# Performance work log

Measured on AMD Instinct MI355X. Metric: run time of the kernel, lower is better.

The kernel has to match this reference:

```python
import jax, jax.numpy as jnp
import numpy as np

B, N, D, H, M, O = 8, 1024, 256, 512, 256, 256


def _mlp(x, W1, b1, W2, b2):
    # two-layer MLP: Linear -> ReLU -> Linear (torch Linear: x @ W.T + b)
    return jax.nn.relu(x @ W1.T + b1) @ W2.T + b2


def _lstm(x, W_ih, W_hh, b):
    # x: [B, N, D] -> h: [B, N, H]; single-layer unidirectional LSTM, torch gate order i,f,g,o
    Bt, Nt, _ = x.shape
    x_proj = x @ W_ih.T + b  # [B, N, 4H] precompute input projection

    def step(carry, xt):
        h, c = carry
        gates = xt + h @ W_hh.T
        i, f, g, o = jnp.split(gates, 4, axis=-1)
        i, f, o = jax.nn.sigmoid(i), jax.nn.sigmoid(f), jax.nn.sigmoid(o)
        c = f * c + i * jnp.tanh(g)
        h = o * jnp.tanh(c)
        return (h, c), h

    h0 = jnp.zeros((Bt, W_hh.shape[1]), x.dtype)
    (_, _), hs = jax.lax.scan(step, (h0, h0), jnp.swapaxes(x_proj, 0, 1))
    return jnp.swapaxes(hs, 0, 1)


def setup_inputs() -> dict:
    key = jax.random.key(0)
    ks = jax.random.split(key, 32)
    p = lambda k, s: jax.random.normal(k, s, jnp.float32) * 0.02
    inp = {
        "feats": jax.random.normal(ks[0], (B, N, D), jnp.float32),
        "adj": jax.random.randint(ks[1], (B, N, N), 0, 2, jnp.int32),
        "W_ih": p(ks[2], (4 * H, D)),
        "W_hh": p(ks[3], (4 * H, H)),
        "b_ih": jnp.zeros((4 * H,), jnp.float32),
        "b_hh": jnp.zeros((4 * H,), jnp.float32),
        "gx_W1": p(ks[4], (M, H)), "gx_b1": jnp.zeros((M,), jnp.float32),
        "gx_W2": p(ks[5], (M, M)), "gx_b2": jnp.zeros((M,), jnp.float32),
        "gz_W1": p(ks[6], (M, H)), "gz_b1": jnp.zeros((M,), jnp.float32),
        "gz_W2": p(ks[7], (M, M)), "gz_b2": jnp.zeros((M,), jnp.float32),
        "gv_W1": p(ks[8], (M, H)), "gv_b1": jnp.zeros((M,), jnp.float32),
        "gv_W2": p(ks[9], (M, M)), "gv_b2": jnp.zeros((M,), jnp.float32),
        "gn_W1": p(ks[10], (M, M)), "gn_b1": jnp.zeros((M,), jnp.float32),
        "gn_W2": p(ks[11], (O, M)), "gn_b2": jnp.zeros((O,), jnp.float32),
        "out_W": p(ks[12], (O, H + O)), "out_b": jnp.zeros((O,), jnp.float32),
    }
    return inp


def reference(feats, adj, W_ih, W_hh, b_ih, b_hh,
              gx_W1, gx_b1, gx_W2, gx_b2,
              gz_W1, gz_b1, gz_W2, gz_b2,
              gv_W1, gv_b1, gv_W2, gv_b2,
              gn_W1, gn_b1, gn_W2, gn_b2,
              out_W, out_b):
    h = _lstm(feats, W_ih, W_hh, b_ih + b_hh)  # [B, N, H]

    # Note: in the source, concat_1[:, :lstm_hidden_dim] == s_i and
    # concat_2[:, :lstm_hidden_dim] == s_j, so scores = <g_x(s_i), g_v(s_j)>
    ax = _mlp(h, gx_W1, gx_b1, gx_W2, gx_b2)  # [B, N, M]
    av = _mlp(h, gv_W1, gv_b1, gv_W2, gv_b2)  # [B, N, M]
    scores = jnp.einsum('bim,bjm->bij', ax, av)  # [B, N, N]

    eye = jnp.eye(N, dtype=bool)
    mask = (adj > 0) & ~eye[None]  # valid neighbors
    w = jax.nn.softmax(jnp.where(mask, scores, -1e30), axis=-1)
    w = w * mask  # zero out rows with no neighbors (softmax of all -inf -> uniform)

    sagg = jnp.einsum('bij,bjh->bih', w, h)  # weighted neighbor sum [B, N, H]
    agg = _mlp(_mlp(sagg, gz_W1, gz_b1, gz_W2, gz_b2), gn_W1, gn_b1, gn_W2, gn_b2)
    has_nb = mask.any(axis=-1, keepdims=True)  # [B, N, 1]
    agg = jnp.where(has_nb, agg, 0.0)  # isolated nodes get zero aggregate

    combined = jnp.concatenate([h, agg], axis=-1)  # [B, N, H+O]
    return combined @ out_W.T + out_b
```

## Files before the change

### kernel.cpp

```cpp
#include <hip/hip_runtime.h>

typedef unsigned short u16;
typedef unsigned long long u64;
using short8 = __attribute__((ext_vector_type(8))) short;
using f32x4  = __attribute__((ext_vector_type(4))) float;

#define GF_RELU  1
#define GF_F32   2
#define GF_XPOSE 4

__device__ __forceinline__ float b2f(u16 x) {
    unsigned u = ((unsigned)x) << 16;
    return __builtin_bit_cast(float, u);
}
__device__ __forceinline__ u16 f2b(float f) {
    unsigned u = __builtin_bit_cast(unsigned, f);
    unsigned r = u + 0x7FFFu + ((u >> 16) & 1u);
    return (u16)(r >> 16);
}
__device__ __forceinline__ f32x4 mfma_bf16(uint4 a, uint4 b, f32x4 c) {
    return __builtin_amdgcn_mfma_f32_16x16x32_bf16(
        __builtin_bit_cast(short8, a), __builtin_bit_cast(short8, b), c, 0, 0, 0);
}
__device__ __forceinline__ f32x4 zero4() { f32x4 z = {0.f, 0.f, 0.f, 0.f}; return z; }

__global__ __launch_bounds__(256) void cvt_bf16(const float* __restrict__ src,
                                                u16* __restrict__ dst, int n) {
    for (int i = blockIdx.x * 256 + threadIdx.x; i < n; i += gridDim.x * 256)
        dst[i] = f2b(src[i]);
}

__global__ void pack_params(const float* __restrict__ Whh, const float* __restrict__ Wih,
                            const float* __restrict__ bih, const float* __restrict__ bhh,
                            u16* __restrict__ WhhP, u16* __restrict__ WihP,
                            float* __restrict__ biasP) {
    int p = blockIdx.x;
    int t = threadIdx.x;
    int orig = ((p & 3) << 9) + (p >> 2);
    WhhP[((long)p << 9) + t]       = f2b(Whh[((long)orig << 9) + t]);
    WhhP[((long)p << 9) + 256 + t] = f2b(Whh[((long)orig << 9) + 256 + t]);
    WihP[((long)p << 8) + t]       = f2b(Wih[((long)orig << 8) + t]);
    if (t == 0) biasP[p] = bih[orig] + bhh[orig];
}

__global__ __launch_bounds__(256) void gemm_bt(
    const u16* __restrict__ A, const u16* __restrict__ A2, int ksplit,
    const u16* __restrict__ B, void* __restrict__ Cout,
    int M, int N, int K,
    long sAb, long sBb, long sCb,
    const float* __restrict__ bias, const float* __restrict__ rowmask, int flags) {
    __shared__ __align__(16) u16 As[64][40];
    __shared__ __align__(16) u16 Bs[128][40];
    const int bz = blockIdx.z;
    const u16* Ab = A + (long)bz * sAb;
    const u16* Bb = B + (long)bz * sBb;
    const int m0 = blockIdx.x << 6, n0 = blockIdx.y << 7;
    const int tid = threadIdx.x;
    const int lane = tid & 63, wave = tid >> 6;
    const int srow = tid >> 2, skc = (tid & 3) << 3;
    const int frm = lane & 15, fq = lane >> 4;

    auto loadA = [&](int ka) -> uint4 {
        const u16* p = (ka < ksplit)
            ? Ab + (long)(m0 + srow) * ksplit + ka
            : A2 + (long)(m0 + srow) * (K - ksplit) + (ka - ksplit);
        return *(const uint4*)p;
    };
    const u16* Brow0 = Bb + (long)(n0 + srow) * K;
    const u16* Brow1 = Bb + (long)(n0 + 64 + srow) * K;

    f32x4 acc[8];
#pragma unroll
    for (int i = 0; i < 8; i++) acc[i] = zero4();

    uint4 a  = loadA(skc);
    uint4 b0 = *(const uint4*)(Brow0 + skc);
    uint4 b1 = *(const uint4*)(Brow1 + skc);

    for (int k0 = 0; k0 < K; k0 += 32) {
        __syncthreads();
        *(uint4*)&As[srow][skc] = a;
        *(uint4*)&Bs[srow][skc] = b0;
        *(uint4*)&Bs[64 + srow][skc] = b1;
        __syncthreads();
        int kn = k0 + 32;
        if (kn < K) {
            a  = loadA(kn + skc);
            b0 = *(const uint4*)(Brow0 + kn + skc);
            b1 = *(const uint4*)(Brow1 + kn + skc);
        }
        uint4 af = *(const uint4*)&As[(wave << 4) + frm][fq << 3];
#pragma unroll
        for (int nt = 0; nt < 8; nt++) {
            uint4 bf = *(const uint4*)&Bs[(nt << 4) + frm][fq << 3];
            acc[nt] = mfma_bf16(af, bf, acc[nt]);
        }
    }
#pragma unroll
    for (int nt = 0; nt < 8; nt++) {
        int col = n0 + (nt << 4) + frm;
        float bv = bias ? bias[col] : 0.f;
#pragma unroll
        for (int r = 0; r < 4; r++) {
            int row = m0 + (wave << 4) + (fq << 2) + r;
            float v = acc[nt][r] + bv;
            if (flags & GF_RELU) v = fmaxf(v, 0.f);
            if (rowmask) v *= rowmask[row];
            long orow = (flags & GF_XPOSE) ? (long)((row & 1023) * 8 + (row >> 10))
                                           : (long)row;
            if (flags & GF_F32)
                ((float*)Cout)[(long)bz * sCb + orow * N + col] = v;
            else
                ((u16*)Cout)[(long)bz * sCb + orow * N + col] = f2b(v);
        }
    }
}

__global__ __launch_bounds__(512, 1) void lstm_rec(
    const u16* __restrict__ WhhP, const u16* __restrict__ xproj,
    u16* __restrict__ h, u64* __restrict__ hx) {
    __shared__ __align__(16) unsigned hshare[8][256];
    const int bid = blockIdx.x;
    const int g = bid & 7;
    const int s = bid >> 3;
    const int tid = threadIdx.x;
    const int lane = tid & 63, wv = tid >> 6;
    const int frm = lane & 15, fq = lane >> 4;
    const int colbase = (s << 8) + (wv << 5);

    uint4 bfrag[2][16];
#pragma unroll
    for (int T = 0; T < 2; T++)
#pragma unroll
        for (int kk = 0; kk < 16; kk++)
            bfrag[T][kk] = *(const uint4*)&WhhP[((long)(colbase + (T << 4) + frm) << 9) +
                                                (kk << 5) + (fq << 3)];

    unsigned* hw = &hshare[wv][0];
    float creg = 0.f;
    int budget = 1 << 20;

#pragma unroll 1
    for (int t = 0; t < 1024; t++) {
        float xp0 = b2f(xproj[((long)(t * 8 + g) << 11) + colbase + frm]);
        float xp1 = b2f(xproj[((long)(t * 8 + g) << 11) + colbase + 16 + frm]);

        float s0, s1;
        if (t > 0) {
            const u64* buf = hx + (g << 9) + (((t - 1) & 1) << 8);
            const u64* p0 = buf + lane;
            const u64* p1 = buf + 64 + lane;
            const u64* p2 = buf + 128 + lane;
            const u64* p3 = buf + 192 + lane;
            u64 v0, v1, v2, v3;
            const unsigned want = (unsigned)t;
            while (true) {
                asm volatile(
                    "global_load_dwordx2 %0, %4, off sc0 sc1\n\t"
                    "global_load_dwordx2 %1, %5, off sc0 sc1\n\t"
                    "global_load_dwordx2 %2, %6, off sc0 sc1\n\t"
                    "global_load_dwordx2 %3, %7, off sc0 sc1\n\t"
                    "s_waitcnt vmcnt(0)"
                    : "=&v"(v0), "=&v"(v1), "=&v"(v2), "=&v"(v3)
                    : "v"(p0), "v"(p1), "v"(p2), "v"(p3)
                    : "memory");
                bool ok = ((unsigned)(v0 >> 32) == want) &
                          ((unsigned)(v1 >> 32) == want) &
                          ((unsigned)(v2 >> 32) == want) &
                          ((unsigned)(v3 >> 32) == want);
                if (__all(ok) || --budget < 0) break;
            }
            hw[lane]       = (unsigned)v0;
            hw[64 + lane]  = (unsigned)v1;
            hw[128 + lane] = (unsigned)v2;
            hw[192 + lane] = (unsigned)v3;

            f32x4 a0p[4], a1p[4];
#pragma unroll
            for (int r = 0; r < 4; r++) { a0p[r] = zero4(); a1p[r] = zero4(); }
#pragma unroll
            for (int r4 = 0; r4 < 4; r4++) {
                uint4 af[4];
#pragma unroll
                for (int q = 0; q < 4; q++)
                    af[q] = *(const uint4*)&hw[(((r4 << 2) | q) << 4) + (fq << 2)];
#pragma unroll
                for (int q = 0; q < 4; q++) {
                    a0p[r4] = mfma_bf16(af[q], bfrag[0][(r4 << 2) | q], a0p[r4]);
                    a1p[r4] = mfma_bf16(af[q], bfrag[1][(r4 << 2) | q], a1p[r4]);
                }
            }
            s0 = (a0p[0][0] + a0p[1][0]) + (a0p[2][0] + a0p[3][0]) + xp0;
            s1 = (a1p[0][0] + a1p[1][0]) + (a1p[2][0] + a1p[3][0]) + xp1;
        } else {
            s0 = xp0;
            s1 = xp1;
        }

        float ss[4];
#pragma unroll
        for (int k = 0; k < 4; k++) {
            int src = ((lane << 2) + k) & 15;
            float t0 = __shfl(s0, src);
            float t1 = __shfl(s1, src);
            ss[k] = (lane < 4) ? t0 : t1;
        }
        float iv = 1.f / (1.f + __expf(-ss[0]));
        float fv = 1.f / (1.f + __expf(-ss[1]));
        float gv = 1.f - 2.f / (__expf(2.f * ss[2]) + 1.f);
        float ov = 1.f / (1.f + __expf(-ss[3]));
        creg = fv * creg + iv * gv;
        float hv = ov * (1.f - 2.f / (__expf(2.f * creg) + 1.f));
        float hn = __shfl_down(hv, 1);
        if (lane < 8 && !(lane & 1)) {
            unsigned dw = (unsigned)f2b(hv) | ((unsigned)f2b(hn) << 16);
            int d = (s << 5) + (wv << 2) + (lane >> 1);
            u64 pv = ((u64)(unsigned)(t + 1) << 32) | (u64)dw;
            u64* dst = &hx[(g << 9) + ((t & 1) << 8) + d];
            asm volatile("global_store_dwordx2 %0, %1, off sc0 sc1"
                         :: "v"(dst), "v"(pv) : "memory");
            ((unsigned*)h)[(((long)(g * 1024 + t)) << 8) + d] = dw;
        }
    }
}

__global__ __launch_bounds__(256) void transpose_h(const u16* __restrict__ h,
                                                   u16* __restrict__ hT) {
    __shared__ __align__(16) u16 tile[64][72];
    const int b = blockIdx.z;
    const int t0 = blockIdx.x << 6, u0 = blockIdx.y << 6;
    const int tid = threadIdx.x;
    const int r = tid >> 3, c8 = (tid & 7) << 3;
#pragma unroll
    for (int j = 0; j < 2; j++) {
        int row = r + (j << 5);
        *(uint4*)&tile[row][c8] =
            *(const uint4*)&h[(((long)b << 10) + t0 + row) * 512 + u0 + c8];
    }
    __syncthreads();
#pragma unroll
    for (int j = 0; j < 2; j++) {
        int urow = r + (j << 5);
        unsigned wds[4];
#pragma unroll
        for (int k = 0; k < 4; k++) {
            unsigned lo = tile[c8 + (k << 1)][urow];
            unsigned hi = tile[c8 + (k << 1) + 1][urow];
            wds[k] = lo | (hi << 16);
        }
        uint4 v; v.x = wds[0]; v.y = wds[1]; v.z = wds[2]; v.w = wds[3];
        *(uint4*)&hT[(((long)b << 9) + u0 + urow) * 1024 + t0 + c8] = v;
    }
}

__global__ __launch_bounds__(256) void softmax_row(
    const float* __restrict__ scores, const int* __restrict__ adj,
    u16* __restrict__ w, float* __restrict__ hasnb) {
    __shared__ float red[4];
    const int row = blockIdx.x;
    const int i = row & 1023;
    const int tid = threadIdx.x;
    const int lane = tid & 63, wave = tid >> 6;
    const float* s = scores + ((long)row << 10);
    const int* arow = adj + ((long)row << 10);

    float sv[4]; bool mk[4];
    float mx = -3.0e38f;
#pragma unroll
    for (int q = 0; q < 4; q++) {
        int j = tid + (q << 8);
        mk[q] = (arow[j] > 0) && (j != i);
        sv[q] = s[j];
        if (mk[q]) mx = fmaxf(mx, sv[q]);
    }
    for (int off = 32; off; off >>= 1) mx = fmaxf(mx, __shfl_xor(mx, off));
    if (lane == 0) red[wave] = mx;
    __syncthreads();
    mx = fmaxf(fmaxf(red[0], red[1]), fmaxf(red[2], red[3]));
    float e[4]; float sum = 0.f;
#pragma unroll
    for (int q = 0; q < 4; q++) {
        e[q] = mk[q] ? __expf(sv[q] - mx) : 0.f;
        sum += e[q];
    }
    __syncthreads();
    for (int off = 32; off; off >>= 1) sum += __shfl_xor(sum, off);
    if (lane == 0) red[wave] = sum;
    __syncthreads();
    sum = red[0] + red[1] + red[2] + red[3];
    float inv = sum > 0.f ? 1.f / sum : 0.f;
#pragma unroll
    for (int q = 0; q < 4; q++) {
        int j = tid + (q << 8);
        w[((long)row << 10) + j] = f2b(e[q] * inv);
    }
    if (tid == 0) hasnb[row] = sum > 0.f ? 1.f : 0.f;
}

extern "C" void kernel_launch(void* const* d_in, const int* in_sizes, int n_in,
                              void* d_out, int out_size, void* d_ws, size_t ws_size,
                              hipStream_t stream) {
    const float* feats = (const float*)d_in[0];
    const int*   adj   = (const int*)d_in[1];
    const float* W_ih  = (const float*)d_in[2];
    const float* W_hh  = (const float*)d_in[3];
    const float* b_ih  = (const float*)d_in[4];
    const float* b_hh  = (const float*)d_in[5];
    const float* gx_W1 = (const float*)d_in[6];  const float* gx_b1 = (const float*)d_in[7];
    const float* gx_W2 = (const float*)d_in[8];  const float* gx_b2 = (const float*)d_in[9];
    const float* gz_W1 = (const float*)d_in[10]; const float* gz_b1 = (const float*)d_in[11];
    const float* gz_W2 = (const float*)d_in[12]; const float* gz_b2 = (const float*)d_in[13];
    const float* gv_W1 = (const float*)d_in[14]; const float* gv_b1 = (const float*)d_in[15];
    const float* gv_W2 = (const float*)d_in[16]; const float* gv_b2 = (const float*)d_in[17];
    const float* gn_W1 = (const float*)d_in[18]; const float* gn_b1 = (const float*)d_in[19];
    const float* gn_W2 = (const float*)d_in[20]; const float* gn_b2 = (const float*)d_in[21];
    const float* out_W = (const float*)d_in[22]; const float* out_b = (const float*)d_in[23];

    char* ws = (char*)d_ws;
    size_t off = 0;
    auto alloc = [&](size_t bytes) {
        void* p = ws + off;
        off += (bytes + 255) & ~(size_t)255;
        return p;
    };
    u16* WhhP      = (u16*)alloc(2048L * 512 * 2);
    u16* WihP      = (u16*)alloc(2048L * 256 * 2);
    float* biasP   = (float*)alloc(2048L * 4);
    u64* hx        = (u64*)alloc(8L * 512 * 8);
    u16* featsB    = (u16*)alloc(8192L * 256 * 2);
    u16* gxW1b     = (u16*)alloc(256L * 512 * 2);
    u16* gxW2b     = (u16*)alloc(256L * 256 * 2);
    u16* gvW1b     = (u16*)alloc(256L * 512 * 2);
    u16* gvW2b     = (u16*)alloc(256L * 256 * 2);
    u16* gzW1b     = (u16*)alloc(256L * 512 * 2);
    u16* gzW2b     = (u16*)alloc(256L * 256 * 2);
    u16* gnW1b     = (u16*)alloc(256L * 256 * 2);
    u16* gnW2b     = (u16*)alloc(256L * 256 * 2);
    u16* outWb     = (u16*)alloc(256L * 768 * 2);
    u16* xproj     = (u16*)alloc(8L * 1024 * 2048 * 2);
    u16* h         = (u16*)alloc(8L * 1024 * 512 * 2);
    u16* hT        = (u16*)alloc(8L * 1024 * 512 * 2);
    u16* t1        = (u16*)alloc(8192L * 256 * 2);
    u16* tB        = (u16*)alloc(8192L * 256 * 2);
    u16* ax        = (u16*)alloc(8192L * 256 * 2);
    u16* av        = (u16*)alloc(8192L * 256 * 2);
    u16* agg       = (u16*)alloc(8192L * 256 * 2);
    float* hasnb   = (float*)alloc(8192L * 4);
    float* scores  = (float*)alloc(8L * 1024 * 1024 * 4);
    u16* w         = (u16*)alloc(8L * 1024 * 1024 * 2);
    if (off > ws_size) return;

    hipMemsetAsync(hx, 0, 8L * 512 * 8, stream);
    pack_params<<<2048, 256, 0, stream>>>(W_hh, W_ih, b_ih, b_hh, WhhP, WihP, biasP);

    auto cvt = [&](const float* src, u16* dst, int n) {
        cvt_bf16<<<(n + 1023) / 1024, 256, 0, stream>>>(src, dst, n);
    };
    cvt(feats, featsB, 8192 * 256);
    cvt(gx_W1, gxW1b, 256 * 512);  cvt(gx_W2, gxW2b, 256 * 256);
    cvt(gv_W1, gvW1b, 256 * 512);  cvt(gv_W2, gvW2b, 256 * 256);
    cvt(gz_W1, gzW1b, 256 * 512);  cvt(gz_W2, gzW2b, 256 * 256);
    cvt(gn_W1, gnW1b, 256 * 256);  cvt(gn_W2, gnW2b, 256 * 256);
    cvt(out_W, outWb, 256 * 768);

    gemm_bt<<<dim3(128, 16, 1), 256, 0, stream>>>(
        featsB, nullptr, 256, WihP, xproj, 8192, 2048, 256, 0, 0, 0,
        biasP, nullptr, GF_XPOSE);

    lstm_rec<<<64, 512, 0, stream>>>(WhhP, xproj, h, hx);

    transpose_h<<<dim3(16, 8, 8), 256, 0, stream>>>(h, hT);

    gemm_bt<<<dim3(128, 2, 1), 256, 0, stream>>>(
        h, nullptr, 512, gxW1b, t1, 8192, 256, 512, 0, 0, 0, gx_b1, nullptr, GF_RELU);
    gemm_bt<<<dim3(128, 2, 1), 256, 0, stream>>>(
        t1, nullptr, 256, gxW2b, ax, 8192, 256, 256, 0, 0, 0, gx_b2, nullptr, 0);
    gemm_bt<<<dim3(128, 2, 1), 256, 0, stream>>>(
        h, nullptr, 512, gvW1b, t1, 8192, 256, 512, 0, 0, 0, gv_b1, nullptr, GF_RELU);
    gemm_bt<<<dim3(128, 2, 1), 256, 0, stream>>>(
        t1, nullptr, 256, gvW2b, av, 8192, 256, 256, 0, 0, 0, gv_b2, nullptr, 0);

    gemm_bt<<<dim3(16, 8, 8), 256, 0, stream>>>(
        ax, nullptr, 256, av, scores, 1024, 1024, 256,
        262144, 262144, 1048576, nullptr, nullptr, GF_F32);

    softmax_row<<<8192, 256, 0, stream>>>(scores, adj, w, hasnb);

    u16* sagg = xproj;
    gemm_bt<<<dim3(16, 4, 8), 256, 0, stream>>>(
        w, nullptr, 1024, hT, sagg, 1024, 512, 1024,
        1048576, 524288, 524288, nullptr, nullptr, 0);

    gemm_bt<<<dim3(128, 2, 1), 256, 0, stream>>>(
        sagg, nullptr, 512, gzW1b, t1, 8192, 256, 512, 0, 0, 0, gz_b1, nullptr, GF_RELU);
    gemm_bt<<<dim3(128, 2, 1), 256, 0, stream>>>(
        t1, nullptr, 256, gzW2b, tB, 8192, 256, 256, 0, 0, 0, gz_b2, nullptr, 0);
    gemm_bt<<<dim3(128, 2, 1), 256, 0, stream>>>(
        tB, nullptr, 256, gnW1b, t1, 8192, 256, 256, 0, 0, 0, gn_b1, nullptr, GF_RELU);
    gemm_bt<<<dim3(128, 2, 1), 256, 0, stream>>>(
        t1, nullptr, 256, gnW2b, agg, 8192, 256, 256, 0, 0, 0, gn_b2, hasnb, 0);

    gemm_bt<<<dim3(128, 2, 1), 256, 0, stream>>>(
        h, agg, 512, outWb, (float*)d_out, 8192, 256, 768, 0, 0, 0, out_b, nullptr, GF_F32);
}
```

Baseline: 2.535 ms.

## Gate LSTM step handoff on per-group arrival counters and prefetch next xproj

Adds a per-group, per-parity arrival counter. Each of the 8 blocks in a batch group atomically increments it after storing its hidden-state slice, and consumers spin on one counter word before reading the tagged h buffer, instead of all lanes repeatedly polling 4 dwordx2 loads. It also hoists the next timestep's input-projection loads to after the step so their latency overlaps the wait. The cost is an extra s_waitcnt plus __syncthreads and an atomic per step on the serial critical path, while the original tag-checking poll is kept as a fallback.

```diff
diff --git a/kernel.cpp b/kernel.cpp
--- a/kernel.cpp
+++ b/kernel.cpp
@@ -118,7 +118,7 @@
 
 __global__ __launch_bounds__(512, 1) void lstm_rec(
     const u16* __restrict__ WhhP, const u16* __restrict__ xproj,
-    u16* __restrict__ h, u64* __restrict__ hx) {
+    u16* __restrict__ h, u64* __restrict__ hx, unsigned* __restrict__ cnt) {
     __shared__ __align__(16) unsigned hshare[8][256];
     const int bid = blockIdx.x;
     const int g = bid & 7;
@@ -137,23 +137,33 @@
                                                 (kk << 5) + (fq << 3)];
 
     unsigned* hw = &hshare[wv][0];
+    unsigned* cbase = cnt + (g << 5);
     float creg = 0.f;
     int budget = 1 << 20;
+    unsigned wantA = 8, wantB = 8;
+
+    float xp0 = b2f(xproj[((long)g << 11) + colbase + frm]);
+    float xp1 = b2f(xproj[((long)g << 11) + colbase + 16 + frm]);
 
 #pragma unroll 1
     for (int t = 0; t < 1024; t++) {
-        float xp0 = b2f(xproj[((long)(t * 8 + g) << 11) + colbase + frm]);
-        float xp1 = b2f(xproj[((long)(t * 8 + g) << 11) + colbase + 16 + frm]);
-
         float s0, s1;
         if (t > 0) {
-            const u64* buf = hx + (g << 9) + (((t - 1) & 1) << 8);
+            const int p2 = (t - 1) & 1;
+            const unsigned want = p2 ? wantB : wantA;
+            if (p2) wantB += 8; else wantA += 8;
+            const unsigned* cp = cbase + p2;
+            while (__hip_atomic_load(cp, __ATOMIC_RELAXED,
+                                     __HIP_MEMORY_SCOPE_AGENT) < want) {
+                if (--budget < 0) break;
+            }
+            const u64* buf = hx + (g << 9) + (p2 << 8);
             const u64* p0 = buf + lane;
             const u64* p1 = buf + 64 + lane;
-            const u64* p2 = buf + 128 + lane;
+            const u64* p2p = buf + 128 + lane;
             const u64* p3 = buf + 192 + lane;
             u64 v0, v1, v2, v3;
-            const unsigned want = (unsigned)t;
+            const unsigned want_t = (unsigned)t;
             while (true) {
                 asm volatile(
                     "global_load_dwordx2 %0, %4, off sc0 sc1\n\t"
@@ -162,12 +172,12 @@
                     "global_load_dwordx2 %3, %7, off sc0 sc1\n\t"
                     "s_waitcnt vmcnt(0)"
                     : "=&v"(v0), "=&v"(v1), "=&v"(v2), "=&v"(v3)
-                    : "v"(p0), "v"(p1), "v"(p2), "v"(p3)
+                    : "v"(p0), "v"(p1), "v"(p2p), "v"(p3)
                     : "memory");
-                bool ok = ((unsigned)(v0 >> 32) == want) &
-                          ((unsigned)(v1 >> 32) == want) &
-                          ((unsigned)(v2 >> 32) == want) &
-                          ((unsigned)(v3 >> 32) == want);
+                bool ok = ((unsigned)(v0 >> 32) == want_t) &
+                          ((unsigned)(v1 >> 32) == want_t) &
+                          ((unsigned)(v2 >> 32) == want_t) &
+                          ((unsigned)(v3 >> 32) == want_t);
                 if (__all(ok) || --budget < 0) break;
             }
             hw[lane]       = (unsigned)v0;
@@ -220,6 +230,15 @@
             asm volatile("global_store_dwordx2 %0, %1, off sc0 sc1"
                          :: "v"(dst), "v"(pv) : "memory");
             ((unsigned*)h)[(((long)(g * 1024 + t)) << 8) + d] = dw;
+        }
+        asm volatile("s_waitcnt vmcnt(0)" ::: "memory");
+        __syncthreads();
+        if (tid == 0)
+            __hip_atomic_fetch_add(&cnt[(g << 5) + (t & 1)], 1u,
+                                   __ATOMIC_RELAXED, __HIP_MEMORY_SCOPE_AGENT);
+        if (t < 1023) {
+            xp0 = b2f(xproj[((long)((t + 1) * 8 + g) << 11) + colbase + frm]);
+            xp1 = b2f(xproj[((long)((t + 1) * 8 + g) << 11) + colbase + 16 + frm]);
         }
     }
 }
@@ -327,6 +346,7 @@
     u16* WihP      = (u16*)alloc(2048L * 256 * 2);
     float* biasP   = (float*)alloc(2048L * 4);
     u64* hx        = (u64*)alloc(8L * 512 * 8);
+    unsigned* cnt  = (unsigned*)alloc(8L * 32 * 4);
     u16* featsB    = (u16*)alloc(8192L * 256 * 2);
     u16* gxW1b     = (u16*)alloc(256L * 512 * 2);
     u16* gxW2b     = (u16*)alloc(256L * 256 * 2);
@@ -351,6 +371,7 @@
     if (off > ws_size) return;
 
     hipMemsetAsync(hx, 0, 8L * 512 * 8, stream);
+    hipMemsetAsync(cnt, 0, 8L * 32 * 4, stream);
     pack_params<<<2048, 256, 0, stream>>>(W_hh, W_ih, b_ih, b_hh, WhhP, WihP, biasP);
 
     auto cvt = [&](const float* src, u16* dst, int n) {
@@ -367,7 +388,7 @@
         featsB, nullptr, 256, WihP, xproj, 8192, 2048, 256, 0, 0, 0,
         biasP, nullptr, GF_XPOSE);
 
-    lstm_rec<<<64, 512, 0, stream>>>(WhhP, xproj, h, hx);
+    lstm_rec<<<64, 512, 0, stream>>>(WhhP, xproj, h, hx, cnt);
 
     transpose_h<<<dim3(16, 8, 8), 256, 0, stream>>>(h, hT);
 
```

Result: slower. 2.861 ms (+12.9%).

## Poll LSTM hidden state with one wave and use L2-scoped atomics when co-located

Applied to the files above, without the earlier changes.

The recurrent LSTM kernel now has only wave 0 poll the global hidden-state exchange buffer. It writes the values to LDS and raises a workgroup flag that the other waves spin on, where before all eight waves polled independently. At startup each block records its XCD id and checks whether the blocks sharing its batch group run on the same XCD. If they do, it polls and publishes through L2-coherent atomics that skip the system-scope cache bypass. This aims to cut per-step cross-block synchronization latency and global traffic, but adds an LDS handoff step and a startup handshake that spins on global memory.

```diff
diff --git a/kernel.cpp b/kernel.cpp
--- a/kernel.cpp
+++ b/kernel.cpp
@@ -116,27 +116,11 @@
     }
 }
 
-__global__ __launch_bounds__(512, 1) void lstm_rec(
-    const u16* __restrict__ WhhP, const u16* __restrict__ xproj,
-    u16* __restrict__ h, u64* __restrict__ hx) {
-    __shared__ __align__(16) unsigned hshare[8][256];
-    const int bid = blockIdx.x;
-    const int g = bid & 7;
-    const int s = bid >> 3;
-    const int tid = threadIdx.x;
-    const int lane = tid & 63, wv = tid >> 6;
-    const int frm = lane & 15, fq = lane >> 4;
-    const int colbase = (s << 8) + (wv << 5);
-
-    uint4 bfrag[2][16];
-#pragma unroll
-    for (int T = 0; T < 2; T++)
-#pragma unroll
-        for (int kk = 0; kk < 16; kk++)
-            bfrag[T][kk] = *(const uint4*)&WhhP[((long)(colbase + (T << 4) + frm) << 9) +
-                                                (kk << 5) + (fq << 3)];
-
-    unsigned* hw = &hshare[wv][0];
+template<bool L2C>
+__device__ __forceinline__ void lstm_loop(
+    const u16* __restrict__ xproj, u16* __restrict__ h, u64* __restrict__ hx,
+    const uint4 (&bfrag)[2][16], unsigned* hsh, int* hflag,
+    int g, int s, int wv, int lane, int frm, int fq, int colbase) {
     float creg = 0.f;
     int budget = 1 << 20;
 
@@ -147,33 +131,58 @@
 
         float s0, s1;
         if (t > 0) {
-            const u64* buf = hx + (g << 9) + (((t - 1) & 1) << 8);
-            const u64* p0 = buf + lane;
-            const u64* p1 = buf + 64 + lane;
-            const u64* p2 = buf + 128 + lane;
-            const u64* p3 = buf + 192 + lane;
-            u64 v0, v1, v2, v3;
-            const unsigned want = (unsigned)t;
-            while (true) {
-                asm volatile(
-                    "global_load_dwordx2 %0, %4, off sc0 sc1\n\t"
-                    "global_load_dwordx2 %1, %5, off sc0 sc1\n\t"
-                    "global_load_dwordx2 %2, %6, off sc0 sc1\n\t"
-                    "global_load_dwordx2 %3, %7, off sc0 sc1\n\t"
-                    "s_waitcnt vmcnt(0)"
-                    : "=&v"(v0), "=&v"(v1), "=&v"(v2), "=&v"(v3)
-                    : "v"(p0), "v"(p1), "v"(p2), "v"(p3)
-                    : "memory");
-                bool ok = ((unsigned)(v0 >> 32) == want) &
-                          ((unsigned)(v1 >> 32) == want) &
-                          ((unsigned)(v2 >> 32) == want) &
-                          ((unsigned)(v3 >> 32) == want);
-                if (__all(ok) || --budget < 0) break;
+            if (wv == 0) {
+                const u64* buf = hx + (g << 9) + (((t - 1) & 1) << 8);
+                const u64* p0 = buf + lane;
+                const u64* p1 = buf + 64 + lane;
+                const u64* p2 = buf + 128 + lane;
+                const u64* p3 = buf + 192 + lane;
+                u64 v0, v1, v2, v3;
+                const unsigned want = (unsigned)t;
+                while (true) {
+                    if constexpr (L2C) {
+                        u64 z = 0;
+                        asm volatile(
+                            "global_atomic_add_x2 %0, %4, %8, off sc0\n\t"
+                            "global_atomic_add_x2 %1, %5, %8, off sc0\n\t"
+                            "global_atomic_add_x2 %2, %6, %8, off sc0\n\t"
+                            "global_atomic_add_x2 %3, %7, %8, off sc0\n\t"
+                            "s_waitcnt vmcnt(0)"
+                            : "=&v"(v0), "=&v"(v1), "=&v"(v2), "=&v"(v3)
+                            : "v"(p0), "v"(p1), "v"(p2), "v"(p3), "v"(z)
+                            : "memory");
+                    } else {
+                        asm volatile(
+                            "global_load_dwordx2 %0, %4, off sc0 sc1\n\t"
+                            "global_load_dwordx2 %1, %5, off sc0 sc1\n\t"
+                            "global_load_dwordx2 %2, %6, off sc0 sc1\n\t"
+                            "global_load_dwordx2 %3, %7, off sc0 sc1\n\t"
+                            "s_waitcnt vmcnt(0)"
+                            : "=&v"(v0), "=&v"(v1), "=&v"(v2), "=&v"(v3)
+                            : "v"(p0), "v"(p1), "v"(p2), "v"(p3)
+                            : "memory");
+                    }
+                    bool ok = ((unsigned)(v0 >> 32) == want) &
+                              ((unsigned)(v1 >> 32) == want) &
+                              ((unsigned)(v2 >> 32) == want) &
+                              ((unsigned)(v3 >> 32) == want);
+                    if (__all(ok) || --budget < 0) break;
+                }
+                hsh[lane]       = (unsigned)v0;
+                hsh[64 + lane]  = (unsigned)v1;
+                hsh[128 + lane] = (unsigned)v2;
+                hsh[192 + lane] = (unsigned)v3;
+                __threadfence_block();
+                if (lane == 0)
+                    __hip_atomic_store(hflag, t, __ATOMIC_RELAXED,
+                                       __HIP_MEMORY_SCOPE_WORKGROUP);
+            } else {
+                while (__hip_atomic_load(hflag, __ATOMIC_RELAXED,
+                                         __HIP_MEMORY_SCOPE_WORKGROUP) < t) {
+                    if (--budget < 0) break;
+                }
+                __threadfence_block();
             }
-            hw[lane]       = (unsigned)v0;
-            hw[64 + lane]  = (unsigned)v1;
-            hw[128 + lane] = (unsigned)v2;
-            hw[192 + lane] = (unsigned)v3;
 
             f32x4 a0p[4], a1p[4];
 #pragma unroll
@@ -183,7 +192,7 @@
                 uint4 af[4];
 #pragma unroll
                 for (int q = 0; q < 4; q++)
-                    af[q] = *(const uint4*)&hw[(((r4 << 2) | q) << 4) + (fq << 2)];
+                    af[q] = *(const uint4*)&hsh[(((r4 << 2) | q) << 4) + (fq << 2)];
 #pragma unroll
                 for (int q = 0; q < 4; q++) {
                     a0p[r4] = mfma_bf16(af[q], bfrag[0][(r4 << 2) | q], a0p[r4]);
@@ -217,11 +226,64 @@
             int d = (s << 5) + (wv << 2) + (lane >> 1);
             u64 pv = ((u64)(unsigned)(t + 1) << 32) | (u64)dw;
             u64* dst = &hx[(g << 9) + ((t & 1) << 8) + d];
-            asm volatile("global_store_dwordx2 %0, %1, off sc0 sc1"
-                         :: "v"(dst), "v"(pv) : "memory");
+            if constexpr (L2C) {
+                asm volatile("global_atomic_swap_x2 %0, %1, off"
+                             :: "v"(dst), "v"(pv) : "memory");
+            } else {
+                asm volatile("global_store_dwordx2 %0, %1, off sc0 sc1"
+                             :: "v"(dst), "v"(pv) : "memory");
+            }
             ((unsigned*)h)[(((long)(g * 1024 + t)) << 8) + d] = dw;
         }
     }
+}
+
+__global__ __launch_bounds__(512, 1) void lstm_rec(
+    const u16* __restrict__ WhhP, const u16* __restrict__ xproj,
+    u16* __restrict__ h, u64* __restrict__ hx, unsigned* __restrict__ xcdid) {
+    __shared__ __align__(16) unsigned hshare[256];
+    __shared__ int hflag;
+    const int bid = blockIdx.x;
+    const int g = bid & 7;
+    const int s = bid >> 3;
+    const int tid = threadIdx.x;
+    const int lane = tid & 63, wv = tid >> 6;
+    const int frm = lane & 15, fq = lane >> 4;
+    const int colbase = (s << 8) + (wv << 5);
+
+    uint4 bfrag[2][16];
+#pragma unroll
+    for (int T = 0; T < 2; T++)
+#pragma unroll
+        for (int kk = 0; kk < 16; kk++)
+            bfrag[T][kk] = *(const uint4*)&WhhP[((long)(colbase + (T << 4) + frm) << 9) +
+                                                (kk << 5) + (fq << 3)];
+
+    unsigned myxcd;
+    asm volatile("s_getreg_b32 %0, hwreg(HW_REG_XCC_ID)" : "=s"(myxcd));
+    if (tid == 0) {
+        hflag = -1;
+        unsigned val = 0x100u | (myxcd & 0xffu);
+        asm volatile("global_store_dword %0, %1, off sc0 sc1"
+                     :: "v"(&xcdid[bid]), "v"(val) : "memory");
+    }
+    const unsigned* pid = &xcdid[g + ((lane & 7) << 3)];
+    unsigned idv = 0;
+    int bd = 1 << 22;
+    while (true) {
+        asm volatile("global_load_dword %0, %1, off sc0 sc1\n\ts_waitcnt vmcnt(0)"
+                     : "=&v"(idv) : "v"(pid) : "memory");
+        if (__all((idv >> 8) == 1u) || --bd < 0) break;
+    }
+    bool same = (bd >= 0) && __all((idv & 0xffu) == (__shfl(idv, 0) & 0xffu));
+    __syncthreads();
+
+    if (same)
+        lstm_loop<true>(xproj, h, hx, bfrag, hshare, &hflag,
+                        g, s, wv, lane, frm, fq, colbase);
+    else
+        lstm_loop<false>(xproj, h, hx, bfrag, hshare, &hflag,
+                         g, s, wv, lane, frm, fq, colbase);
 }
 
 __global__ __launch_bounds__(256) void transpose_h(const u16* __restrict__ h,
@@ -327,6 +389,7 @@
     u16* WihP      = (u16*)alloc(2048L * 256 * 2);
     float* biasP   = (float*)alloc(2048L * 4);
     u64* hx        = (u64*)alloc(8L * 512 * 8);
+    unsigned* xcdid = (unsigned*)alloc(64L * 4);
     u16* featsB    = (u16*)alloc(8192L * 256 * 2);
     u16* gxW1b     = (u16*)alloc(256L * 512 * 2);
     u16* gxW2b     = (u16*)alloc(256L * 256 * 2);
@@ -351,6 +414,7 @@
     if (off > ws_size) return;
 
     hipMemsetAsync(hx, 0, 8L * 512 * 8, stream);
+    hipMemsetAsync(xcdid, 0, 64L * 4, stream);
     pack_params<<<2048, 256, 0, stream>>>(W_hh, W_ih, b_ih, b_hh, WhhP, WihP, biasP);
 
     auto cvt = [&](const float* src, u16* dst, int n) {
@@ -367,7 +431,7 @@
         featsB, nullptr, 256, WihP, xproj, 8192, 2048, 256, 0, 0, 0,
         biasP, nullptr, GF_XPOSE);
 
-    lstm_rec<<<64, 512, 0, stream>>>(WhhP, xproj, h, hx);
+    lstm_rec<<<64, 512, 0, stream>>>(WhhP, xproj, h, hx, xcdid);
 
     transpose_h<<<dim3(16, 8, 8), 256, 0, stream>>>(h, hT);
 
```

Result: faster. 2.422 ms (-4.4%).
